# Performance work log

Hardware: AMD Instinct MI355X
Metric: run time of the kernel (lower is better)

Reference implementation:

```python
import jax, jax.numpy as jnp
import numpy as np

N_NODES = 50000
N_EDGES = 800000
IN_DIM = 128
HIDDEN = 128
NUM_CLASSES = 2
NUM_GRAPHS = 512


def _linear_params(key, fan_in, fan_out):
    # torch nn.Linear default init: U(-1/sqrt(fan_in), 1/sqrt(fan_in))
    k1, k2 = jax.random.split(key)
    bound = 1.0 / np.sqrt(fan_in)
    W = jax.random.uniform(k1, (fan_in, fan_out), jnp.float32, -bound, bound)
    b = jax.random.uniform(k2, (fan_out,), jnp.float32, -bound, bound)
    return W, b


def setup_inputs() -> dict:
    key = jax.random.key(0)
    ks = jax.random.split(key, 8)
    x = jax.random.normal(ks[0], (N_NODES, IN_DIM), jnp.float32)
    edge_index = jax.random.randint(ks[1], (2, N_EDGES), 0, N_NODES, jnp.int64)
    batch = jnp.sort(jax.random.randint(ks[2], (N_NODES,), 0, NUM_GRAPHS, jnp.int64))
    W1a, b1a = _linear_params(ks[3], IN_DIM, HIDDEN)
    W1b, b1b = _linear_params(ks[4], HIDDEN, HIDDEN)
    W2a, b2a = _linear_params(ks[5], HIDDEN, HIDDEN)
    W2b, b2b = _linear_params(ks[6], HIDDEN, HIDDEN)
    Wfc, bfc = _linear_params(ks[7], HIDDEN, NUM_CLASSES)
    return {"x": x, "edge_index": edge_index, "batch": batch,
            "W1a": W1a, "b1a": b1a, "W1b": W1b, "b1b": b1b,
            "W2a": W2a, "b2a": b2a, "W2b": W2b, "b2b": b2b,
            "Wfc": Wfc, "bfc": bfc}


def _gin_layer(x, src, dst, Wa, ba, Wb, bb):
    # GINConv (eps=0): h_i = MLP(x_i + sum_{j->i} x_j)
    agg = jax.ops.segment_sum(x[src], dst, num_segments=N_NODES)
    h = x + agg
    h = jax.nn.relu(h @ Wa + ba)
    h = h @ Wb + bb
    return jax.nn.relu(h)  # outer F.relu in forward; dropout is identity (eval)


def reference(x, edge_index, batch, W1a, b1a, W1b, b1b, W2a, b2a, W2b, b2b, Wfc, bfc):
    src, dst = edge_index[0], edge_index[1]
    h = _gin_layer(x, src, dst, W1a, b1a, W1b, b1b)
    h = _gin_layer(h, src, dst, W2a, b2a, W2b, b2b)
    # global mean pool per graph
    sums = jax.ops.segment_sum(h, batch, num_segments=NUM_GRAPHS)
    counts = jax.ops.segment_sum(jnp.ones((N_NODES,), h.dtype), batch, num_segments=NUM_GRAPHS)
    g_emb = sums / jnp.maximum(counts, 1.0)[:, None]
    return g_emb @ Wfc + bfc  # [NUM_GRAPHS, NUM_CLASSES]
```

## Files before the change

### kernel.cpp

```cpp
#include <hip/hip_runtime.h>

typedef unsigned short ushort_t;
typedef unsigned int uint_t;

typedef __bf16 bf16x8 __attribute__((ext_vector_type(8)));
typedef float f32x4 __attribute__((ext_vector_type(4)));

#define N_NODES 50000
#define N_EDGES 800000
#define DIM 128
#define NUM_GRAPHS 512
#define LDA 136

#define ELL_CAP 64

#define NBUCK 256
#define BUCK_SZ 196
#define LROW 66
#define FIFO_CAP 4096
#define A_CHUNK 2048
#define A_BLOCKS ((N_EDGES + A_CHUNK - 1) / A_CHUNK)

#define PREP_X_BLOCKS 6250
#define PREP_W_BLOCKS 256
#define PREP_B_BLOCKS 196
#define PREP_TOTAL (A_BLOCKS + PREP_X_BLOCKS + PREP_W_BLOCKS + PREP_B_BLOCKS + 1)

__device__ __forceinline__ float bf2f(ushort_t u) {
    return __uint_as_float(((uint_t)u) << 16);
}
__device__ __forceinline__ ushort_t f2bf(float f) {
    uint_t u = __float_as_uint(f);
    u = (u + 0x7FFF + ((u >> 16) & 1)) >> 16;
    return (ushort_t)u;
}
__device__ __forceinline__ bf16x8 as_bf16x8(uint4 v) {
    return __builtin_bit_cast(bf16x8, v);
}

__global__ void zero_detect_kernel(int* gcnt, const void* xraw,
                                   const void* eiraw, int* flags) {
    int i = threadIdx.x;
    if (i < NBUCK) gcnt[i] = 0;
    if (i == 0) {
        const ushort_t* u = (const ushort_t*)xraw;
        int extreme = 0;
        for (int k = 0; k < 128; ++k) {
            int e = (u[k] >> 7) & 0xFF;
            if (e >= 0xC0) extreme++;
        }
        flags[0] = (extreme > 8) ? 1 : 0;
        const int* p = (const int*)eiraw;
        int nonzero = 0;
        for (int k = 1; k < 64; k += 2) nonzero += (p[k] != 0);
        flags[1] = (nonzero == 0) ? 1 : 0;
    }
}

__global__ __launch_bounds__(256) void prep_all_kernel(
    const void* xraw, const void* braw, const void* eiraw,
    const void* W0, const void* W1, const void* W2, const void* W3,
    const void* pb1a, const void* pb1b, const void* pb2a, const void* pb2b,
    const void* pWfc, const void* pbfc, const int* __restrict__ flags,
    ushort_t* __restrict__ xout, ushort_t* __restrict__ wpout,
    int* __restrict__ batch32, float* __restrict__ params,
    int* __restrict__ gcnt, uint_t* __restrict__ fifo) {
    __shared__ int lcnt[NBUCK];
    __shared__ int lbase[NBUCK];
    int b = blockIdx.x;
    int tid = threadIdx.x;
    if (b < A_BLOCKS) {
        lcnt[tid] = 0;
        __syncthreads();
        const int* p = (const int*)eiraw;
        int i64 = flags[1];
        int base_e = b * A_CHUNK;
        int gk[8], rk[8];
        uint_t pk[8];
#pragma unroll
        for (int k = 0; k < 8; ++k) {
            int e = base_e + k * 256 + tid;
            int valid = e < N_EDGES;
            int s = 0, d = 0;
            if (valid) {
                if (i64) { s = p[2 * e]; d = p[2 * (N_EDGES + e)]; }
                else     { s = p[e];     d = p[N_EDGES + e]; }
            }
            int g = d / BUCK_SZ;
            gk[k] = valid ? g : -1;
            pk[k] = (uint_t)s | ((uint_t)(d - g * BUCK_SZ) << 16);
            rk[k] = valid ? atomicAdd(&lcnt[g], 1) : 0;
        }
        __syncthreads();
        lbase[tid] = atomicAdd(&gcnt[tid], lcnt[tid]);
        __syncthreads();
#pragma unroll
        for (int k = 0; k < 8; ++k) {
            if (gk[k] >= 0) {
                int pos = lbase[gk[k]] + rk[k];
                if (pos < FIFO_CAP)
                    fifo[(size_t)gk[k] * FIFO_CAP + pos] = pk[k];
            }
        }
    } else if (b < A_BLOCKS + PREP_X_BLOCKS) {
        if (flags[0]) {
            int i = (b - A_BLOCKS) * 256 + tid;
            if (i < N_NODES * DIM / 4) {
                float4 v = ((const float4*)xraw)[i];
                ushort4 o;
                o.x = f2bf(v.x); o.y = f2bf(v.y); o.z = f2bf(v.z); o.w = f2bf(v.w);
                ((ushort4*)xout)[i] = o;
            }
        }
    } else if (b < A_BLOCKS + PREP_X_BLOCKS + PREP_W_BLOCKS) {
        int gidx = (b - A_BLOCKS - PREP_X_BLOCKS) * 256 + tid;
        int which = gidx >> 14;
        const void* W = (which == 0) ? W0 : (which == 1) ? W1 : (which == 2) ? W2 : W3;
        int idx = gidx & 16383;
        int j = idx & 7;
        int L = (idx >> 3) & 63;
        int t = (idx >> 9) & 7;
        int s = idx >> 12;
        int k = s * 32 + (L >> 4) * 8 + j;
        int n = t * 16 + (L & 15);
        int off = k * DIM + n;
        wpout[gidx] = flags[0] ? f2bf(((const float*)W)[off]) : ((const ushort_t*)W)[off];
    } else if (b < A_BLOCKS + PREP_X_BLOCKS + PREP_W_BLOCKS + PREP_B_BLOCKS) {
        int i = (b - A_BLOCKS - PREP_X_BLOCKS - PREP_W_BLOCKS) * 256 + tid;
        if (i < N_NODES) {
            const int* p = (const int*)braw;
            batch32[i] = flags[1] ? p[2 * i] : p[i];
        }
    } else {
        for (int i = tid; i < 770; i += 256) {
            const void* srcp;
            int j;
            if (i < 128)      { srcp = pb1a; j = i; }
            else if (i < 256) { srcp = pb1b; j = i - 128; }
            else if (i < 384) { srcp = pb2a; j = i - 256; }
            else if (i < 512) { srcp = pb2b; j = i - 384; }
            else if (i < 768) { srcp = pWfc; j = i - 512; }
            else              { srcp = pbfc; j = i - 768; }
            params[i] = flags[0] ? ((const float*)srcp)[j] : bf2f(((const ushort_t*)srcp)[j]);
        }
    }
}

__global__ __launch_bounds__(256) void scatter_kernel(const uint_t* __restrict__ fifo,
                                                      const int* __restrict__ gcnt,
                                                      int* __restrict__ cnt,
                                                      ushort_t* __restrict__ ell,
                                                      float* __restrict__ gsum) {
    __shared__ ushort_t lell[BUCK_SZ][LROW];
    __shared__ int lcnt[BUCK_SZ];
    int b = blockIdx.x;
    int tid = threadIdx.x;
    gsum[b * 256 + tid] = 0.f;
    if (tid < BUCK_SZ) lcnt[tid] = 0;
    int n = gcnt[b];
    if (n > FIFO_CAP) n = FIFO_CAP;
    const uint_t* f = fifo + (size_t)b * FIFO_CAP;
    uint_t ebuf[16];
#pragma unroll
    for (int k = 0; k < 16; ++k) {
        int i = k * 256 + tid;
        ebuf[k] = (i < n) ? f[i] : 0xFFFFFFFFu;
    }
    __syncthreads();
    for (int band = 0; band < 13; ++band) {
#pragma unroll
        for (int k = 0; k < 16; ++k) {
            uint_t e = ebuf[k];
            int src = (int)(e & 0xFFFFu);
            if ((src >> 12) == band) {
                int dl = (int)(e >> 16);
                int slot = atomicAdd(&lcnt[dl], 1);
                if (slot < ELL_CAP) lell[dl][slot] = (ushort_t)src;
            }
        }
        __syncthreads();
    }
    int node0 = b * BUCK_SZ;
    uint_t* __restrict__ ell32 = (uint_t*)ell;
    for (int i = tid; i < BUCK_SZ * (ELL_CAP / 2); i += 256) {
        int dl = i >> 5;
        int u = i & 31;
        int node = node0 + dl;
        if (node < N_NODES)
            ell32[(size_t)node * (ELL_CAP / 2) + u] =
                *reinterpret_cast<const uint_t*>(&lell[dl][2 * u]);
    }
    if (tid < BUCK_SZ) {
        int node = node0 + tid;
        if (node < N_NODES) {
            int deg = lcnt[tid];
            cnt[node] = (deg > ELL_CAP) ? ELL_CAP : deg;
        }
    }
}

__global__ __launch_bounds__(256) void agg_kernel(const ushort_t* __restrict__ featA,
                                                  const void* __restrict__ featB,
                                                  const int* __restrict__ flags,
                                                  const int* __restrict__ deg,
                                                  const ushort_t* __restrict__ ell,
                                                  ushort_t* __restrict__ hout) {
    int n = blockIdx.x * 16 + (threadIdx.x >> 4);
    int lane = threadIdx.x & 15;
    if (n >= N_NODES) return;
    const ushort_t* feat = featA;
    if (flags && !flags[0]) feat = (const ushort_t*)featB;
    const uint4* fp = reinterpret_cast<const uint4*>(feat);
    uint4 v = fp[(size_t)n * 16 + lane];
    float a0 = bf2f((ushort_t)(v.x & 0xffff));
    float a1 = bf2f((ushort_t)(v.x >> 16));
    float a2 = bf2f((ushort_t)(v.y & 0xffff));
    float a3 = bf2f((ushort_t)(v.y >> 16));
    float a4 = bf2f((ushort_t)(v.z & 0xffff));
    float a5 = bf2f((ushort_t)(v.z >> 16));
    float a6 = bf2f((ushort_t)(v.w & 0xffff));
    float a7 = bf2f((ushort_t)(v.w >> 16));
    int e1 = deg[n];
    const uint4* __restrict__ rp4 = reinterpret_cast<const uint4*>(ell + (size_t)n * ELL_CAP);
    const ushort_t* __restrict__ row = ell + (size_t)n * ELL_CAP;
    int j = 0;
#define ACC8(V) \
    a0 += bf2f((ushort_t)((V).x & 0xffff)); a1 += bf2f((ushort_t)((V).x >> 16)); \
    a2 += bf2f((ushort_t)((V).y & 0xffff)); a3 += bf2f((ushort_t)((V).y >> 16)); \
    a4 += bf2f((ushort_t)((V).z & 0xffff)); a5 += bf2f((ushort_t)((V).z >> 16)); \
    a6 += bf2f((ushort_t)((V).w & 0xffff)); a7 += bf2f((ushort_t)((V).w >> 16));
    for (; j + 8 <= e1; j += 8) {
        uint4 ra = rp4[j >> 3];
        int s0 = (int)(ra.x & 0xffff), s1 = (int)(ra.x >> 16);
        int s2 = (int)(ra.y & 0xffff), s3 = (int)(ra.y >> 16);
        int s4 = (int)(ra.z & 0xffff), s5 = (int)(ra.z >> 16);
        int s6 = (int)(ra.w & 0xffff), s7 = (int)(ra.w >> 16);
        uint4 g0 = fp[(size_t)s0 * 16 + lane];
        uint4 g1 = fp[(size_t)s1 * 16 + lane];
        uint4 g2 = fp[(size_t)s2 * 16 + lane];
        uint4 g3 = fp[(size_t)s3 * 16 + lane];
        uint4 g4 = fp[(size_t)s4 * 16 + lane];
        uint4 g5 = fp[(size_t)s5 * 16 + lane];
        uint4 g6 = fp[(size_t)s6 * 16 + lane];
        uint4 g7 = fp[(size_t)s7 * 16 + lane];
        ACC8(g0) ACC8(g1) ACC8(g2) ACC8(g3)
        ACC8(g4) ACC8(g5) ACC8(g6) ACC8(g7)
    }
    if (j + 4 <= e1) {
        uint2 ra = *reinterpret_cast<const uint2*>(row + j);
        int s0 = (int)(ra.x & 0xffff), s1 = (int)(ra.x >> 16);
        int s2 = (int)(ra.y & 0xffff), s3 = (int)(ra.y >> 16);
        uint4 g0 = fp[(size_t)s0 * 16 + lane];
        uint4 g1 = fp[(size_t)s1 * 16 + lane];
        uint4 g2 = fp[(size_t)s2 * 16 + lane];
        uint4 g3 = fp[(size_t)s3 * 16 + lane];
        ACC8(g0) ACC8(g1) ACC8(g2) ACC8(g3)
        j += 4;
    }
    for (; j < e1; ++j) {
        int s = (int)row[j];
        uint4 g0 = fp[(size_t)s * 16 + lane];
        ACC8(g0)
    }
#undef ACC8
    uint4 o;
    o.x = (uint_t)f2bf(a0) | ((uint_t)f2bf(a1) << 16);
    o.y = (uint_t)f2bf(a2) | ((uint_t)f2bf(a3) << 16);
    o.z = (uint_t)f2bf(a4) | ((uint_t)f2bf(a5) << 16);
    o.w = (uint_t)f2bf(a6) | ((uint_t)f2bf(a7) << 16);
    reinterpret_cast<uint4*>(hout)[(size_t)n * 16 + lane] = o;
}

__global__ __launch_bounds__(256) void mlp_kernel(const ushort_t* __restrict__ hin,
                                                  const ushort_t* __restrict__ wpA,
                                                  const float* __restrict__ ba,
                                                  const ushort_t* __restrict__ wpB,
                                                  const float* __restrict__ bb,
                                                  ushort_t* __restrict__ hout) {
    __shared__ ushort_t As[64 * LDA];
    int tid = threadIdx.x;
    int wave = tid >> 6;
    int lane = tid & 63;
    int quad = lane >> 4;
    int cl = lane & 15;
    int row0 = blockIdx.x * 64;

    bf16x8 B1[2][4], B2[2][4];
#pragma unroll
    for (int ti = 0; ti < 2; ++ti) {
        int t = 2 * wave + ti;
#pragma unroll
        for (int s = 0; s < 4; ++s) {
            B1[ti][s] = as_bf16x8(reinterpret_cast<const uint4*>(wpA)[(s * 8 + t) * 64 + lane]);
            B2[ti][s] = as_bf16x8(reinterpret_cast<const uint4*>(wpB)[(s * 8 + t) * 64 + lane]);
        }
    }

    for (int i = tid; i < 64 * 16; i += 256) {
        int r = i >> 4, c8 = i & 15;
        uint4 v = make_uint4(0u, 0u, 0u, 0u);
        int gr = row0 + r;
        if (gr < N_NODES)
            v = reinterpret_cast<const uint4*>(hin + (size_t)gr * DIM)[c8];
        *reinterpret_cast<uint4*>(&As[r * LDA + c8 * 8]) = v;
    }
    __syncthreads();

    f32x4 acc[4][2];
#pragma unroll
    for (int m = 0; m < 4; ++m)
#pragma unroll
        for (int ti = 0; ti < 2; ++ti)
#pragma unroll
            for (int r = 0; r < 4; ++r) acc[m][ti][r] = 0.f;

#pragma unroll
    for (int s = 0; s < 4; ++s) {
#pragma unroll
        for (int m = 0; m < 4; ++m) {
            bf16x8 a = *reinterpret_cast<const bf16x8*>(&As[(m * 16 + cl) * LDA + s * 32 + quad * 8]);
#pragma unroll
            for (int ti = 0; ti < 2; ++ti)
                acc[m][ti] = __builtin_amdgcn_mfma_f32_16x16x32_bf16(a, B1[ti][s], acc[m][ti], 0, 0, 0);
        }
    }
    __syncthreads();

#pragma unroll
    for (int ti = 0; ti < 2; ++ti) {
        int col = 32 * wave + ti * 16 + cl;
        float bv = ba[col];
#pragma unroll
        for (int m = 0; m < 4; ++m)
#pragma unroll
            for (int r = 0; r < 4; ++r) {
                float v = acc[m][ti][r] + bv;
                As[(m * 16 + quad * 4 + r) * LDA + col] = f2bf(fmaxf(v, 0.f));
            }
    }
    __syncthreads();

#pragma unroll
    for (int m = 0; m < 4; ++m)
#pragma unroll
        for (int ti = 0; ti < 2; ++ti)
#pragma unroll
            for (int r = 0; r < 4; ++r) acc[m][ti][r] = 0.f;

#pragma unroll
    for (int s = 0; s < 4; ++s) {
#pragma unroll
        for (int m = 0; m < 4; ++m) {
            bf16x8 a = *reinterpret_cast<const bf16x8*>(&As[(m * 16 + cl) * LDA + s * 32 + quad * 8]);
#pragma unroll
            for (int ti = 0; ti < 2; ++ti)
                acc[m][ti] = __builtin_amdgcn_mfma_f32_16x16x32_bf16(a, B2[ti][s], acc[m][ti], 0, 0, 0);
        }
    }

#pragma unroll
    for (int ti = 0; ti < 2; ++ti) {
        int col = 32 * wave + ti * 16 + cl;
        float bv = bb[col];
#pragma unroll
        for (int m = 0; m < 4; ++m)
#pragma unroll
            for (int r = 0; r < 4; ++r) {
                int gr = row0 + m * 16 + quad * 4 + r;
                if (gr < N_NODES) {
                    float v = acc[m][ti][r] + bv;
                    hout[(size_t)gr * DIM + col] = f2bf(fmaxf(v, 0.f));
                }
            }
    }
}

__global__ __launch_bounds__(256) void mlp_pool_kernel(const ushort_t* __restrict__ hin,
                                                       const ushort_t* __restrict__ wpA,
                                                       const float* __restrict__ ba,
                                                       const ushort_t* __restrict__ wpB,
                                                       const float* __restrict__ bb,
                                                       const int* __restrict__ batch32,
                                                       float* __restrict__ gsum) {
    __shared__ ushort_t As[64 * LDA];
    int tid = threadIdx.x;
    int wave = tid >> 6;
    int lane = tid & 63;
    int quad = lane >> 4;
    int cl = lane & 15;
    int row0 = blockIdx.x * 64;

    bf16x8 B1[2][4], B2[2][4];
#pragma unroll
    for (int ti = 0; ti < 2; ++ti) {
        int t = 2 * wave + ti;
#pragma unroll
        for (int s = 0; s < 4; ++s) {
            B1[ti][s] = as_bf16x8(reinterpret_cast<const uint4*>(wpA)[(s * 8 + t) * 64 + lane]);
            B2[ti][s] = as_bf16x8(reinterpret_cast<const uint4*>(wpB)[(s * 8 + t) * 64 + lane]);
        }
    }

    for (int i = tid; i < 64 * 16; i += 256) {
        int r = i >> 4, c8 = i & 15;
        uint4 v = make_uint4(0u, 0u, 0u, 0u);
        int gr = row0 + r;
        if (gr < N_NODES)
            v = reinterpret_cast<const uint4*>(hin + (size_t)gr * DIM)[c8];
        *reinterpret_cast<uint4*>(&As[r * LDA + c8 * 8]) = v;
    }
    __syncthreads();

    f32x4 acc[4][2];
#pragma unroll
    for (int m = 0; m < 4; ++m)
#pragma unroll
        for (int ti = 0; ti < 2; ++ti)
#pragma unroll
            for (int r = 0; r < 4; ++r) acc[m][ti][r] = 0.f;

#pragma unroll
    for (int s = 0; s < 4; ++s) {
#pragma unroll
        for (int m = 0; m < 4; ++m) {
            bf16x8 a = *reinterpret_cast<const bf16x8*>(&As[(m * 16 + cl) * LDA + s * 32 + quad * 8]);
#pragma unroll
            for (int ti = 0; ti < 2; ++ti)
                acc[m][ti] = __builtin_amdgcn_mfma_f32_16x16x32_bf16(a, B1[ti][s], acc[m][ti], 0, 0, 0);
        }
    }
    __syncthreads();

#pragma unroll
    for (int ti = 0; ti < 2; ++ti) {
        int col = 32 * wave + ti * 16 + cl;
        float bv = ba[col];
#pragma unroll
        for (int m = 0; m < 4; ++m)
#pragma unroll
            for (int r = 0; r < 4; ++r) {
                float v = acc[m][ti][r] + bv;
                As[(m * 16 + quad * 4 + r) * LDA + col] = f2bf(fmaxf(v, 0.f));
            }
    }
    __syncthreads();

#pragma unroll
    for (int m = 0; m < 4; ++m)
#pragma unroll
        for (int ti = 0; ti < 2; ++ti)
#pragma unroll
            for (int r = 0; r < 4; ++r) acc[m][ti][r] = 0.f;

#pragma unroll
    for (int s = 0; s < 4; ++s) {
#pragma unroll
        for (int m = 0; m < 4; ++m) {
            bf16x8 a = *reinterpret_cast<const bf16x8*>(&As[(m * 16 + cl) * LDA + s * 32 + quad * 8]);
#pragma unroll
            for (int ti = 0; ti < 2; ++ti)
                acc[m][ti] = __builtin_amdgcn_mfma_f32_16x16x32_bf16(a, B2[ti][s], acc[m][ti], 0, 0, 0);
        }
    }
    __syncthreads();

#pragma unroll
    for (int ti = 0; ti < 2; ++ti) {
        int col = 32 * wave + ti * 16 + cl;
        float bv = bb[col];
#pragma unroll
        for (int m = 0; m < 4; ++m)
#pragma unroll
            for (int r = 0; r < 4; ++r) {
                float v = acc[m][ti][r] + bv;
                As[(m * 16 + quad * 4 + r) * LDA + col] = f2bf(fmaxf(v, 0.f));
            }
    }
    __syncthreads();

    int c = tid & 127;
    int rbase = (tid >> 7) * 32;
    float accp = 0.f;
    int curg = -1;
    for (int r = rbase; r < rbase + 32; ++r) {
        int gr = row0 + r;
        if (gr >= N_NODES) break;
        int g = batch32[gr];
        if (g != curg) {
            if (curg >= 0) atomicAdd(&gsum[curg * DIM + c], accp);
            curg = g;
            accp = 0.f;
        }
        accp += bf2f(As[r * LDA + c]);
    }
    if (curg >= 0) atomicAdd(&gsum[curg * DIM + c], accp);
}

__global__ __launch_bounds__(64) void fc_kernel(const float* __restrict__ gsum,
                                                const int* __restrict__ batch,
                                                const float* __restrict__ params,
                                                const int* __restrict__ flags,
                                                void* __restrict__ out) {
    int g = blockIdx.x;
    int l = threadIdx.x;
    int lo = 0, hi = N_NODES;
    while (lo < hi) { int mid = (lo + hi) >> 1; if (batch[mid] < g) lo = mid + 1; else hi = mid; }
    int start = lo;
    hi = N_NODES;
    while (lo < hi) { int mid = (lo + hi) >> 1; if (batch[mid] < g + 1) lo = mid + 1; else hi = mid; }
    int cnt = lo - start;
    float inv = 1.0f / (float)(cnt > 0 ? cnt : 1);
    float m0 = gsum[g * DIM + l] * inv;
    float m1 = gsum[g * DIM + 64 + l] * inv;
    float p0 = m0 * params[512 + l * 2 + 0] + m1 * params[512 + (64 + l) * 2 + 0];
    float p1 = m0 * params[512 + l * 2 + 1] + m1 * params[512 + (64 + l) * 2 + 1];
#pragma unroll
    for (int off = 32; off > 0; off >>= 1) {
        p0 += __shfl_down(p0, off, 64);
        p1 += __shfl_down(p1, off, 64);
    }
    if (l == 0) {
        float o0 = p0 + params[768];
        float o1 = p1 + params[769];
        if (flags[0]) {
            ((float*)out)[g * 2 + 0] = o0;
            ((float*)out)[g * 2 + 1] = o1;
        } else {
            ((ushort_t*)out)[g * 2 + 0] = f2bf(o0);
            ((ushort_t*)out)[g * 2 + 1] = f2bf(o1);
        }
    }
}

extern "C" void kernel_launch(void* const* d_in, const int* in_sizes, int n_in,
                              void* d_out, int out_size, void* d_ws, size_t ws_size,
                              hipStream_t stream) {
    const void* x = d_in[0];
    const void* ei = d_in[1];
    const void* batch = d_in[2];
    const void* W1a = d_in[3];
    const void* b1a = d_in[4];
    const void* W1b = d_in[5];
    const void* b1b = d_in[6];
    const void* W2a = d_in[7];
    const void* b2a = d_in[8];
    const void* W2b = d_in[9];
    const void* b2b = d_in[10];
    const void* Wfc = d_in[11];
    const void* bfc = d_in[12];

    char* base = (char*)d_ws;
    ushort_t* hX = (ushort_t*)base;   base += (size_t)N_NODES * DIM * 2;
    ushort_t* hA = (ushort_t*)base;   base += (size_t)N_NODES * DIM * 2;
    ushort_t* ell = (ushort_t*)base;  base += (size_t)N_NODES * ELL_CAP * 2;
    uint_t* fifo = (uint_t*)base;     base += (size_t)NBUCK * FIFO_CAP * 4;
    int* cnt = (int*)base;            base += (size_t)N_NODES * 4;
    int* batch32 = (int*)base;        base += (size_t)N_NODES * 4;
    int* gcnt = (int*)base;           base += NBUCK * 4;
    ushort_t* wp = (ushort_t*)base;   base += 4 * 16384 * 2;
    float* params = (float*)base;     base += 772 * 4;
    float* gsum = (float*)base;       base += (size_t)NUM_GRAPHS * DIM * 4;
    int* flags = (int*)base;          base += 16;

    ushort_t* wpA1 = wp;
    ushort_t* wpB1 = wp + 16384;
    ushort_t* wpA2 = wp + 2 * 16384;
    ushort_t* wpB2 = wp + 3 * 16384;

    zero_detect_kernel<<<1, 256, 0, stream>>>(gcnt, x, ei, flags);
    prep_all_kernel<<<PREP_TOTAL, 256, 0, stream>>>(x, batch, ei, W1a, W1b, W2a, W2b,
                                                    b1a, b1b, b2a, b2b, Wfc, bfc, flags,
                                                    hX, wp, batch32, params, gcnt, fifo);
    scatter_kernel<<<NBUCK, 256, 0, stream>>>(fifo, gcnt, cnt, ell, gsum);

    agg_kernel<<<(N_NODES + 15) / 16, 256, 0, stream>>>(hX, x, flags, cnt, ell, hA);
    mlp_kernel<<<(N_NODES + 63) / 64, 256, 0, stream>>>(hA, wpA1, params + 0, wpB1, params + 128, hA);
    agg_kernel<<<(N_NODES + 15) / 16, 256, 0, stream>>>(hA, hA, nullptr, cnt, ell, hX);
    mlp_pool_kernel<<<(N_NODES + 63) / 64, 256, 0, stream>>>(hX, wpA2, params + 256, wpB2, params + 384,
                                                             batch32, gsum);
    fc_kernel<<<NUM_GRAPHS, 64, 0, stream>>>(gsum, batch32, params, flags, d_out);
}
```

Before: 234.6 us.

## Use finer destination buckets and a two-pass count/place edge binning

Destination buckets grow from 256 to 1024, each now covering 49 nodes, so the scatter kernel launches 1024 blocks holding fewer edges each. Each edge-binning block now takes 8192 edges and makes two passes: it counts per bucket first, reserves global offsets, then re-reads the edges and places them using shared-memory cursors. The goal is to spread the scatter/ELL build across more blocks and cut per-block register and shared-memory pressure. The cost is that edge indices are read twice, there are fewer binning blocks, and the FIFO cap of 1536 per bucket is tighter and could silently drop edges if a bucket overflows.

```diff
diff --git a/kernel.cpp b/kernel.cpp
--- a/kernel.cpp
+++ b/kernel.cpp
@@ -14,11 +14,11 @@
 
 #define ELL_CAP 64
 
-#define NBUCK 256
-#define BUCK_SZ 196
+#define NBUCK 1024
+#define BUCK_SZ 49
 #define LROW 66
-#define FIFO_CAP 4096
-#define A_CHUNK 2048
+#define FIFO_CAP 1536
+#define A_CHUNK 8192
 #define A_BLOCKS ((N_EDGES + A_CHUNK - 1) / A_CHUNK)
 
 #define PREP_X_BLOCKS 6250
@@ -40,7 +40,7 @@
 
 __global__ void zero_detect_kernel(int* gcnt, const void* xraw,
                                    const void* eiraw, int* flags) {
-    int i = threadIdx.x;
+    int i = blockIdx.x * 256 + threadIdx.x;
     if (i < NBUCK) gcnt[i] = 0;
     if (i == 0) {
         const ushort_t* u = (const ushort_t*)xraw;
@@ -66,41 +66,38 @@
     int* __restrict__ batch32, float* __restrict__ params,
     int* __restrict__ gcnt, uint_t* __restrict__ fifo) {
     __shared__ int lcnt[NBUCK];
-    __shared__ int lbase[NBUCK];
+    __shared__ int lcur[NBUCK];
     int b = blockIdx.x;
     int tid = threadIdx.x;
     if (b < A_BLOCKS) {
-        lcnt[tid] = 0;
+        for (int i = tid; i < NBUCK; i += 256) lcnt[i] = 0;
         __syncthreads();
         const int* p = (const int*)eiraw;
-        int i64 = flags[1];
+        int i64f = flags[1];
         int base_e = b * A_CHUNK;
-        int gk[8], rk[8];
-        uint_t pk[8];
-#pragma unroll
-        for (int k = 0; k < 8; ++k) {
-            int e = base_e + k * 256 + tid;
-            int valid = e < N_EDGES;
-            int s = 0, d = 0;
-            if (valid) {
-                if (i64) { s = p[2 * e]; d = p[2 * (N_EDGES + e)]; }
-                else     { s = p[e];     d = p[N_EDGES + e]; }
-            }
+        int nE = N_EDGES - base_e;
+        if (nE > A_CHUNK) nE = A_CHUNK;
+        for (int i = tid; i < nE; i += 256) {
+            int e = base_e + i;
+            int d = i64f ? p[2 * (N_EDGES + e)] : p[N_EDGES + e];
+            atomicAdd(&lcnt[d / BUCK_SZ], 1);
+        }
+        __syncthreads();
+        for (int i = tid; i < NBUCK; i += 256) {
+            int c = lcnt[i];
+            lcur[i] = c ? atomicAdd(&gcnt[i], c) : 0;
+        }
+        __syncthreads();
+        for (int i = tid; i < nE; i += 256) {
+            int e = base_e + i;
+            int s, d;
+            if (i64f) { s = p[2 * e]; d = p[2 * (N_EDGES + e)]; }
+            else      { s = p[e];     d = p[N_EDGES + e]; }
             int g = d / BUCK_SZ;
-            gk[k] = valid ? g : -1;
-            pk[k] = (uint_t)s | ((uint_t)(d - g * BUCK_SZ) << 16);
-            rk[k] = valid ? atomicAdd(&lcnt[g], 1) : 0;
-        }
-        __syncthreads();
-        lbase[tid] = atomicAdd(&gcnt[tid], lcnt[tid]);
-        __syncthreads();
-#pragma unroll
-        for (int k = 0; k < 8; ++k) {
-            if (gk[k] >= 0) {
-                int pos = lbase[gk[k]] + rk[k];
-                if (pos < FIFO_CAP)
-                    fifo[(size_t)gk[k] * FIFO_CAP + pos] = pk[k];
-            }
+            int pos = atomicAdd(&lcur[g], 1);
+            if (pos < FIFO_CAP)
+                fifo[(size_t)g * FIFO_CAP + pos] =
+                    (uint_t)s | ((uint_t)(d - g * BUCK_SZ) << 16);
         }
     } else if (b < A_BLOCKS + PREP_X_BLOCKS) {
         if (flags[0]) {
@@ -155,21 +152,21 @@
     __shared__ int lcnt[BUCK_SZ];
     int b = blockIdx.x;
     int tid = threadIdx.x;
-    gsum[b * 256 + tid] = 0.f;
+    if (b < 256) gsum[b * 256 + tid] = 0.f;
     if (tid < BUCK_SZ) lcnt[tid] = 0;
     int n = gcnt[b];
     if (n > FIFO_CAP) n = FIFO_CAP;
     const uint_t* f = fifo + (size_t)b * FIFO_CAP;
-    uint_t ebuf[16];
-#pragma unroll
-    for (int k = 0; k < 16; ++k) {
+    uint_t ebuf[6];
+#pragma unroll
+    for (int k = 0; k < 6; ++k) {
         int i = k * 256 + tid;
         ebuf[k] = (i < n) ? f[i] : 0xFFFFFFFFu;
     }
     __syncthreads();
     for (int band = 0; band < 13; ++band) {
 #pragma unroll
-        for (int k = 0; k < 16; ++k) {
+        for (int k = 0; k < 6; ++k) {
             uint_t e = ebuf[k];
             int src = (int)(e & 0xFFFFu);
             if ((src >> 12) == band) {
@@ -567,7 +564,7 @@
     ushort_t* wpA2 = wp + 2 * 16384;
     ushort_t* wpB2 = wp + 3 * 16384;
 
-    zero_detect_kernel<<<1, 256, 0, stream>>>(gcnt, x, ei, flags);
+    zero_detect_kernel<<<(NBUCK + 255) / 256, 256, 0, stream>>>(gcnt, x, ei, flags);
     prep_all_kernel<<<PREP_TOTAL, 256, 0, stream>>>(x, batch, ei, W1a, W1b, W2a, W2b,
                                                     b1a, b1b, b2a, b2b, Wfc, bfc, flags,
                                                     hX, wp, batch32, params, gcnt, fifo);
```

New measurement: 243.2 us. +3.7%, slower.
